# Performance work log

Hardware: AMD Instinct MI355X
Metric: run time of the kernel (lower is better)

The kernel has to match this reference:

```python
import jax, jax.numpy as jnp
import numpy as np

D = 3            # input_ch (pos dims)
L = 16           # n_levels
F = 2            # n_feats per level
LOG2 = 19
CAP = 1 << LOG2  # hashmap capacity per level
COARSEST, FINEST = 16.0, 2048.0
N = 524288
D1 = D + 1
HASH_MULT = np.int32(2531011)


def _elevate_matrix():
    # Linear map R^D -> hyperplane {sum=0} in R^{D+1} (Adams et al. permutohedral lattice)
    sf = 1.0 / np.sqrt(np.arange(1, D + 1, dtype=np.float64) * np.arange(2, D + 2, dtype=np.float64))
    E = np.zeros((D1, D), np.float32)
    E[0, :] = sf
    for i in range(1, D1):
        E[i, i - 1] = -i * sf[i - 1]
        E[i, i:] = sf[i:]
    return E


def _scales():
    g = (FINEST / COARSEST) ** (np.arange(L, dtype=np.float64) / (L - 1))
    return (COARSEST * g).astype(np.float32)


def permuto_forward(pos, params):
    E = jnp.asarray(_elevate_matrix())
    scales = jnp.asarray(_scales())
    x = pos[None] * scales[:, None, None]              # [L,N,D]
    elev = jnp.einsum('vp,lnp->lnv', E, x)             # [L,N,D1]
    # nearest lattice remainder-0 point (multiples of D1)
    rem0f = jnp.round(elev / D1) * D1
    sums = (jnp.sum(rem0f, -1) / D1).astype(jnp.int32)  # exactly integer
    di = elev - rem0f
    # rank[i] = #{j : d_j > d_i  or (d_j == d_i and j < i)}
    gt = di[..., None, :] > di[..., :, None]
    eq = di[..., None, :] == di[..., :, None]
    jlt = jnp.arange(D1)[None, :] < jnp.arange(D1)[:, None]
    rank = jnp.sum(gt | (eq & jlt), -1).astype(jnp.int32) + sums[..., None]
    rem0 = rem0f.astype(jnp.int32)
    under = (rank < 0).astype(jnp.int32)
    over = (rank > D).astype(jnp.int32)
    rank = rank + (under - over) * D1
    rem0 = rem0 + (under - over) * D1
    # barycentric weights of the D1 simplex vertices
    delta = (elev - rem0.astype(elev.dtype)) / D1      # [L,N,D1]
    dbr = jnp.take_along_axis(delta, jnp.argsort(rank, -1), -1)  # delta ordered by rank
    w0 = 1.0 + dbr[..., -1] - dbr[..., 0]
    w = jnp.concatenate([w0[..., None], -(dbr[..., 1:] - dbr[..., :-1])[..., ::-1]], -1)  # [L,N,D1]
    # integer keys of the D1 simplex vertices (first D coords; last is implicit)
    kk = jnp.arange(D1, dtype=jnp.int32)
    keys = (rem0[..., None, :D] + kk[:, None]
            - D1 * (rank[..., None, :D] > (D - kk[:, None])).astype(jnp.int32))  # [L,N,D1,D]
    # hash: k = (k + key_i) * 2531011, wrap in 32 bits, mask to capacity (pow2)
    h = jnp.zeros(keys.shape[:-1], jnp.int32)
    for i in range(D):
        h = (h + keys[..., i]) * HASH_MULT
    idx = h & (CAP - 1)                                # [L,N,D1]
    flat_idx = idx + jnp.arange(L, dtype=jnp.int32)[:, None, None] * CAP
    feats = params.reshape(L * CAP, F)[flat_idx]       # [L,N,D1,F]
    out = jnp.einsum('lnv,lnvf->lnf', w, feats)        # [L,N,F]
    return jnp.moveaxis(out, 0, 1).reshape(pos.shape[0], L * F)


def setup_inputs() -> dict:
    key = jax.random.key(0)
    k1, k2 = jax.random.split(key)
    pos = jax.random.uniform(k1, (N, D), jnp.float32)                 # coords in [0,1)
    params = jax.random.normal(k2, (L * CAP * F,), jnp.float32) * 1e-4  # param_init std
    return {"input": pos, "flattened_params": params}


def reference(input, flattened_params):
    return permuto_forward(input, flattened_params)
```

## Files before the change

kernel.cpp:

```cpp
#include <hip/hip_runtime.h>
#include <hip/hip_fp16.h>
#include <cmath>

namespace {

typedef float    vf4 __attribute__((ext_vector_type(4)));
typedef unsigned uv2 __attribute__((ext_vector_type(2)));

constexpr int kN = 524288;
constexpr int kL = 16;
constexpr int kCapLog2 = 19;
constexpr int kCap = 1 << kCapLog2;
constexpr int kCapMask = kCap - 1;
constexpr unsigned kHashMult = 2531011u;

constexpr int cD[4][3]   = {{ 8, 8, 6},{10,10, 9},{13,12,10},{17,16,14}};
constexpr int cB[4][3]   = {{-4,-16,-16},{-4,-20,-24},{-4,-24,-28},{-4,-32,-40}};
constexpr int cOff[4]    = {0, 1536, 5136, 11376};
constexpr int kLdsCnt    = 11376;
constexpr int kDenseCnt  = 26608;

constexpr int kMegaMain  = 15360;
constexpr int kBuildBlks = 104;
constexpr int kConvBaseF4 = 7 * (kCap * 2 / 4);

struct ScaleArr { float s[kL]; };

__device__ __forceinline__ void permuto_point(
    float x0, float x1, float x2, int rem0[4], int rank[4], float w[4])
{
    const float E00 = (float)( 0.70710678118654752440);
    const float E01 = (float)( 0.40824829046386301637);
    const float E02 = (float)( 0.28867513459481288225);
    const float E10 = (float)(-0.70710678118654752440);
    const float E21 = (float)(-2.0 * 0.40824829046386301637);
    const float E32 = (float)(-3.0 * 0.28867513459481288225);

    float elev[4];
    elev[0] = E00 * x0 + E01 * x1 + E02 * x2;
    elev[1] = E10 * x0 + E01 * x1 + E02 * x2;
    elev[2] =            E21 * x1 + E02 * x2;
    elev[3] =                       E32 * x2;

    float rem0f[4], di[4];
    #pragma unroll
    for (int v = 0; v < 4; ++v) {
        rem0f[v] = rintf(elev[v] * 0.25f) * 4.0f;
        di[v]    = elev[v] - rem0f[v];
    }
    const int sums = (int)((((rem0f[0] + rem0f[1]) + rem0f[2]) + rem0f[3]) * 0.25f);

    #pragma unroll
    for (int a = 0; a < 4; ++a) {
        int r = 0;
        #pragma unroll
        for (int b = 0; b < 4; ++b)
            r += (di[b] > di[a]) || (di[b] == di[a] && b < a);
        rank[a] = r + sums;
        rem0[a] = (int)rem0f[a];
    }
    #pragma unroll
    for (int v = 0; v < 4; ++v) {
        if (rank[v] < 0)      { rank[v] += 4; rem0[v] += 4; }
        else if (rank[v] > 3) { rank[v] -= 4; rem0[v] -= 4; }
    }

    float dbr[4];
    #pragma unroll
    for (int v = 0; v < 4; ++v)
        dbr[rank[v] & 3] = (elev[v] - (float)rem0[v]) * 0.25f;

    w[0] = (1.0f + dbr[3]) - dbr[0];
    w[1] = dbr[2] - dbr[3];
    w[2] = dbr[1] - dbr[2];
    w[3] = dbr[0] - dbr[1];
}

__global__ __launch_bounds__(256) void mega1(
    const float* __restrict__ pos,
    const float* __restrict__ params,
    unsigned* __restrict__ tab,
    unsigned* __restrict__ out_t16,
    unsigned* __restrict__ dense,
    ScaleArr sc)
{
    const int b = blockIdx.x;
    if (b < kMegaMain) {
        const int q = b / 5, r = b % 5;
        if (r < 2) {
            const int idx   = q * 2 + r;
            const int level = 4 + (idx >> 11);
            const int n     = ((idx & 2047) << 8) + threadIdx.x;

            const float s  = sc.s[level];
            const float x0 = __builtin_nontemporal_load(pos + 3 * n + 0) * s;
            const float x1 = __builtin_nontemporal_load(pos + 3 * n + 1) * s;
            const float x2 = __builtin_nontemporal_load(pos + 3 * n + 2) * s;

            int rem0[4], rank[4];
            float w[4];
            permuto_point(x0, x1, x2, rem0, rank, w);

            const float2* __restrict__ t2 =
                (const float2*)params + ((size_t)level << kCapLog2);
            int hidx[4];
            #pragma unroll
            for (int k = 0; k < 4; ++k) {
                int h = 0;
                #pragma unroll
                for (int i = 0; i < 3; ++i) {
                    const int key = rem0[i] + k - 4 * (rank[i] > 3 - k);
                    h = (int)((unsigned)(h + key) * kHashMult);
                }
                hidx[k] = h & kCapMask;
            }
            float2 f[4];
            #pragma unroll
            for (int k = 0; k < 4; ++k) f[k] = t2[hidx[k]];

            float o0 = 0.0f, o1 = 0.0f;
            #pragma unroll
            for (int k = 0; k < 4; ++k) { o0 += w[k] * f[k].x; o1 += w[k] * f[k].y; }

            const __half2 po = __floats2half2_rn(o0, o1);
            __builtin_nontemporal_store(*reinterpret_cast<const unsigned*>(&po),
                                        out_t16 + ((size_t)level << kCapLog2) + n);
        } else {
            const int i  = q * 3 + (r - 2);
            const int jj = kConvBaseF4 + i * 256 + threadIdx.x;
            vf4 v = __builtin_nontemporal_load((const vf4*)params + jj);
            __half2 a = __floats2half2_rn(v.x, v.y);
            __half2 c = __floats2half2_rn(v.z, v.w);
            uv2 o;
            o.x = *reinterpret_cast<unsigned*>(&a);
            o.y = *reinterpret_cast<unsigned*>(&c);
            __builtin_nontemporal_store(o, (uv2*)tab + jj);
        }
    } else {
        const int e = (b - kMegaMain) * 256 + threadIdx.x;
        if (e >= kDenseCnt) return;
        int l, r;
        if      (e < cOff[1]) { l = 0; r = e; }
        else if (e < cOff[2]) { l = 1; r = e - cOff[1]; }
        else if (e < cOff[3]) { l = 2; r = e - cOff[2]; }
        else                  { l = 3; r = e - cOff[3]; }
        const int d0 = cD[l][0], d1 = cD[l][1], d2 = cD[l][2];
        const int per = d0 * d1 * d2;
        int rr = r;
        const int k  = rr / per;  rr -= k * per;
        const int i0 = rr / (d1 * d2); rr -= i0 * (d1 * d2);
        const int i1 = rr / d2;
        const int i2 = rr - i1 * d2;

        const int key0 = cB[l][0] + 4 * i0 + k;
        const int key1 = cB[l][1] + 4 * i1 + k;
        const int key2 = cB[l][2] + 4 * i2 + k;
        int h = 0;
        h = (int)((unsigned)(h + key0) * kHashMult);
        h = (int)((unsigned)(h + key1) * kHashMult);
        h = (int)((unsigned)(h + key2) * kHashMult);
        const size_t entry = ((size_t)l << kCapLog2) + (h & kCapMask);
        const __half2 hv = __floats2half2_rn(params[entry * 2], params[entry * 2 + 1]);
        dense[e] = *reinterpret_cast<const unsigned*>(&hv);
    }
}

__global__ __launch_bounds__(256) void fine715(
    const float* __restrict__ pos,
    const unsigned* __restrict__ tab,
    unsigned* __restrict__ out_t16,
    ScaleArr sc)
{
    const int b   = blockIdx.x;
    const int xcd = b & 7;
    const int j   = b >> 3;
    int level, n;
    if (j < 2048) {
        level = 7 + xcd;
        n = (j << 8) + threadIdx.x;
    } else {
        level = 15;
        const int c = (j - 2048) + (xcd << 8);
        n = (c << 8) + threadIdx.x;
    }

    const float s  = sc.s[level];
    const float x0 = __builtin_nontemporal_load(pos + 3 * n + 0) * s;
    const float x1 = __builtin_nontemporal_load(pos + 3 * n + 1) * s;
    const float x2 = __builtin_nontemporal_load(pos + 3 * n + 2) * s;

    int rem0[4], rank[4];
    float w[4];
    permuto_point(x0, x1, x2, rem0, rank, w);

    const unsigned* __restrict__ t = tab + ((size_t)level << kCapLog2);
    int hidx[4];
    #pragma unroll
    for (int k = 0; k < 4; ++k) {
        int h = 0;
        #pragma unroll
        for (int i = 0; i < 3; ++i) {
            const int key = rem0[i] + k - 4 * (rank[i] > 3 - k);
            h = (int)((unsigned)(h + key) * kHashMult);
        }
        hidx[k] = h & kCapMask;
    }
    unsigned e[4];
    #pragma unroll
    for (int k = 0; k < 4; ++k) e[k] = t[hidx[k]];

    float o0 = 0.0f, o1 = 0.0f;
    #pragma unroll
    for (int k = 0; k < 4; ++k) {
        const __half2 hv = *reinterpret_cast<const __half2*>(&e[k]);
        o0 += w[k] * __low2float(hv);
        o1 += w[k] * __high2float(hv);
    }
    const __half2 po = __floats2half2_rn(o0, o1);
    __builtin_nontemporal_store(*reinterpret_cast<const unsigned*>(&po),
                                out_t16 + ((size_t)level << kCapLog2) + n);
}

__global__ __launch_bounds__(256) void permuto_coarse(
    const float* __restrict__ pos,
    const unsigned* __restrict__ dense,
    unsigned* __restrict__ out_t16,
    ScaleArr sc)
{
    __shared__ unsigned sd[kLdsCnt];
    for (int i = threadIdx.x; i < kLdsCnt; i += 256)
        sd[i] = dense[i];
    __syncthreads();

    const int n = blockIdx.x * 256 + threadIdx.x;
    const float p0 = __builtin_nontemporal_load(pos + 3 * n + 0);
    const float p1 = __builtin_nontemporal_load(pos + 3 * n + 1);
    const float p2 = __builtin_nontemporal_load(pos + 3 * n + 2);
    const unsigned* __restrict__ denseL3 = dense + cOff[3];

    #pragma unroll
    for (int l = 0; l < 4; ++l) {
        const float s = sc.s[l];
        int rem0[4], rank[4];
        float w[4];
        permuto_point(p0 * s, p1 * s, p2 * s, rem0, rank, w);

        unsigned ev[4];
        #pragma unroll
        for (int k = 0; k < 4; ++k) {
            const int i0 = (rem0[0] - 4 * (rank[0] > 3 - k) - cB[l][0]) >> 2;
            const int i1 = (rem0[1] - 4 * (rank[1] > 3 - k) - cB[l][1]) >> 2;
            const int i2 = (rem0[2] - 4 * (rank[2] > 3 - k) - cB[l][2]) >> 2;
            const int idx = ((k * cD[l][0] + i0) * cD[l][1] + i1) * cD[l][2] + i2;
            ev[k] = (l < 3) ? sd[cOff[l] + idx] : denseL3[idx];
        }
        float o0 = 0.0f, o1 = 0.0f;
        #pragma unroll
        for (int k = 0; k < 4; ++k) {
            const __half2 hv = *reinterpret_cast<const __half2*>(&ev[k]);
            o0 += w[k] * __low2float(hv);
            o1 += w[k] * __high2float(hv);
        }
        const __half2 po = __floats2half2_rn(o0, o1);
        __builtin_nontemporal_store(*reinterpret_cast<const unsigned*>(&po),
                                    out_t16 + ((size_t)l << kCapLog2) + n);
    }
}

__global__ __launch_bounds__(256) void transpose_out16(
    const unsigned* __restrict__ out_t16, vf4* __restrict__ out4)
{
    __shared__ float tile[256][36];
    const int t  = threadIdx.x;
    const int p0 = blockIdx.x * 256;

    #pragma unroll
    for (int l = 0; l < kL; ++l) {
        const unsigned u = __builtin_nontemporal_load(out_t16 + ((size_t)l << kCapLog2) + p0 + t);
        const __half2 hv = *reinterpret_cast<const __half2*>(&u);
        tile[t][2 * l + 0] = __low2float(hv);
        tile[t][2 * l + 1] = __high2float(hv);
    }
    __syncthreads();

    const size_t base = (size_t)p0 * 8;
    #pragma unroll
    for (int i = 0; i < 8; ++i) {
        const int idx = i * 256 + t;
        const int p = idx >> 3, q = idx & 7;
        vf4 v = *reinterpret_cast<const vf4*>(&tile[p][4 * q]);
        out4[base + idx] = v;
    }
}

__global__ __launch_bounds__(256) void permuto_fwd(
    const float* __restrict__ pos,
    const float* __restrict__ params,
    float* __restrict__ out,
    ScaleArr sc)
{
    const int gid = blockIdx.x * 256 + threadIdx.x;
    const int l = gid & (kL - 1);
    const int n = gid >> 4;

    const float s  = sc.s[l];
    const float x0 = pos[3 * n + 0] * s;
    const float x1 = pos[3 * n + 1] * s;
    const float x2 = pos[3 * n + 2] * s;

    int rem0[4], rank[4];
    float w[4];
    permuto_point(x0, x1, x2, rem0, rank, w);

    const float2* __restrict__ tab = (const float2*)params + ((size_t)l << kCapLog2);
    float o0 = 0.0f, o1 = 0.0f;
    #pragma unroll
    for (int k = 0; k < 4; ++k) {
        int h = 0;
        #pragma unroll
        for (int i = 0; i < 3; ++i) {
            const int key = rem0[i] + k - 4 * (rank[i] > 3 - k);
            h = (int)((unsigned)(h + key) * kHashMult);
        }
        const float2 f = tab[h & kCapMask];
        o0 += w[k] * f.x;
        o1 += w[k] * f.y;
    }
    ((float2*)out)[(n << 4) + l] = make_float2(o0, o1);
}

}

extern "C" void kernel_launch(void* const* d_in, const int* in_sizes, int n_in,
                              void* d_out, int out_size, void* d_ws, size_t ws_size,
                              hipStream_t stream) {
    const float* pos    = (const float*)d_in[0];
    const float* params = (const float*)d_in[1];
    float* out          = (float*)d_out;

    ScaleArr sc;
    for (int l = 0; l < kL; ++l)
        sc.s[l] = (float)(16.0 * pow(128.0, (double)l / 15.0));

    const size_t tab_bytes   = (size_t)kL * kCap * 4;
    const size_t outt_bytes  = (size_t)kL * kN * 4;
    const size_t dense_bytes = (size_t)kDenseCnt * 4;

    if (ws_size >= tab_bytes + outt_bytes + dense_bytes) {
        unsigned* tab     = (unsigned*)d_ws;
        unsigned* out_t16 = (unsigned*)((char*)d_ws + tab_bytes);
        unsigned* dense   = (unsigned*)((char*)d_ws + tab_bytes + outt_bytes);

        mega1<<<kMegaMain + kBuildBlks, 256, 0, stream>>>(pos, params, tab, out_t16, dense, sc);
        fine715<<<8 * 2304, 256, 0, stream>>>(pos, tab, out_t16, sc);
        permuto_coarse<<<kN / 256, 256, 0, stream>>>(pos, dense, out_t16, sc);
        transpose_out16<<<kN / 256, 256, 0, stream>>>(out_t16, (vf4*)out);
    } else {
        permuto_fwd<<<(kN * kL) / 256, 256, 0, stream>>>(pos, params, out, sc);
    }
}
```

Measured before the change: 175.1 us.

## Split fine gathers into halves and overlap transpose with second-half gathers

The three launches for fine gathers, coarse gathers and transpose become a split by point halves. The first kernel runs the fine levels and coarse levels for the first half plus level 15 for that half. The second kernel runs the fine gathers for the second half alongside the transpose of the first half. A final small kernel transposes the second half. The aim is to overlap the bandwidth-bound transpose with the latency-bound random gathers and to cut tail effects between launches, at the cost of a larger LDS footprint per block in the combined kernels, which could lower occupancy.

New measurement: 177.2 us. Within noise of the previous version (+1.2%).

```diff
diff --git a/kernel.cpp b/kernel.cpp
--- a/kernel.cpp
+++ b/kernel.cpp
@@ -13,6 +13,9 @@
 constexpr int kCap = 1 << kCapLog2;
 constexpr int kCapMask = kCap - 1;
 constexpr unsigned kHashMult = 2531011u;
+
+constexpr int kHalf = kN / 2;
+constexpr int kHB   = kHalf / 256;
 
 constexpr int cD[4][3]   = {{ 8, 8, 6},{10,10, 9},{13,12,10},{17,16,14}};
 constexpr int cB[4][3]   = {{-4,-16,-16},{-4,-20,-24},{-4,-24,-28},{-4,-32,-40}};
@@ -74,6 +77,47 @@
     w[1] = dbr[2] - dbr[3];
     w[2] = dbr[1] - dbr[2];
     w[3] = dbr[0] - dbr[1];
+}
+
+__device__ __forceinline__ void fine_job(
+    const float* __restrict__ pos, const unsigned* __restrict__ tab,
+    unsigned* __restrict__ out_t16, const ScaleArr& sc, int level, int n)
+{
+    const float s  = sc.s[level];
+    const float x0 = __builtin_nontemporal_load(pos + 3 * n + 0) * s;
+    const float x1 = __builtin_nontemporal_load(pos + 3 * n + 1) * s;
+    const float x2 = __builtin_nontemporal_load(pos + 3 * n + 2) * s;
+
+    int rem0[4], rank[4];
+    float w[4];
+    permuto_point(x0, x1, x2, rem0, rank, w);
+
+    const unsigned* __restrict__ t = tab + ((size_t)level << kCapLog2);
+    int hidx[4];
+    #pragma unroll
+    for (int k = 0; k < 4; ++k) {
+        int h = 0;
+        #pragma unroll
+        for (int i = 0; i < 3; ++i) {
+            const int key = rem0[i] + k - 4 * (rank[i] > 3 - k);
+            h = (int)((unsigned)(h + key) * kHashMult);
+        }
+        hidx[k] = h & kCapMask;
+    }
+    unsigned e[4];
+    #pragma unroll
+    for (int k = 0; k < 4; ++k) e[k] = t[hidx[k]];
+
+    float o0 = 0.0f, o1 = 0.0f;
+    #pragma unroll
+    for (int k = 0; k < 4; ++k) {
+        const __half2 hv = *reinterpret_cast<const __half2*>(&e[k]);
+        o0 += w[k] * __low2float(hv);
+        o1 += w[k] * __high2float(hv);
+    }
+    const __half2 po = __floats2half2_rn(o0, o1);
+    __builtin_nontemporal_store(*reinterpret_cast<const unsigned*>(&po),
+                                out_t16 + ((size_t)level << kCapLog2) + n);
 }
 
 __global__ __launch_bounds__(256) void mega1(
@@ -165,114 +209,72 @@
     }
 }
 
-__global__ __launch_bounds__(256) void fine715(
+__global__ __launch_bounds__(256) void gather_a(
     const float* __restrict__ pos,
     const unsigned* __restrict__ tab,
-    unsigned* __restrict__ out_t16,
-    ScaleArr sc)
-{
-    const int b   = blockIdx.x;
-    const int xcd = b & 7;
-    const int j   = b >> 3;
-    int level, n;
-    if (j < 2048) {
-        level = 7 + xcd;
-        n = (j << 8) + threadIdx.x;
-    } else {
-        level = 15;
-        const int c = (j - 2048) + (xcd << 8);
-        n = (c << 8) + threadIdx.x;
-    }
-
-    const float s  = sc.s[level];
-    const float x0 = __builtin_nontemporal_load(pos + 3 * n + 0) * s;
-    const float x1 = __builtin_nontemporal_load(pos + 3 * n + 1) * s;
-    const float x2 = __builtin_nontemporal_load(pos + 3 * n + 2) * s;
-
-    int rem0[4], rank[4];
-    float w[4];
-    permuto_point(x0, x1, x2, rem0, rank, w);
-
-    const unsigned* __restrict__ t = tab + ((size_t)level << kCapLog2);
-    int hidx[4];
-    #pragma unroll
-    for (int k = 0; k < 4; ++k) {
-        int h = 0;
-        #pragma unroll
-        for (int i = 0; i < 3; ++i) {
-            const int key = rem0[i] + k - 4 * (rank[i] > 3 - k);
-            h = (int)((unsigned)(h + key) * kHashMult);
-        }
-        hidx[k] = h & kCapMask;
-    }
-    unsigned e[4];
-    #pragma unroll
-    for (int k = 0; k < 4; ++k) e[k] = t[hidx[k]];
-
-    float o0 = 0.0f, o1 = 0.0f;
-    #pragma unroll
-    for (int k = 0; k < 4; ++k) {
-        const __half2 hv = *reinterpret_cast<const __half2*>(&e[k]);
-        o0 += w[k] * __low2float(hv);
-        o1 += w[k] * __high2float(hv);
-    }
-    const __half2 po = __floats2half2_rn(o0, o1);
-    __builtin_nontemporal_store(*reinterpret_cast<const unsigned*>(&po),
-                                out_t16 + ((size_t)level << kCapLog2) + n);
-}
-
-__global__ __launch_bounds__(256) void permuto_coarse(
-    const float* __restrict__ pos,
     const unsigned* __restrict__ dense,
     unsigned* __restrict__ out_t16,
     ScaleArr sc)
 {
-    __shared__ unsigned sd[kLdsCnt];
-    for (int i = threadIdx.x; i < kLdsCnt; i += 256)
-        sd[i] = dense[i];
-    __syncthreads();
-
-    const int n = blockIdx.x * 256 + threadIdx.x;
-    const float p0 = __builtin_nontemporal_load(pos + 3 * n + 0);
-    const float p1 = __builtin_nontemporal_load(pos + 3 * n + 1);
-    const float p2 = __builtin_nontemporal_load(pos + 3 * n + 2);
-    const unsigned* __restrict__ denseL3 = dense + cOff[3];
-
-    #pragma unroll
-    for (int l = 0; l < 4; ++l) {
-        const float s = sc.s[l];
-        int rem0[4], rank[4];
-        float w[4];
-        permuto_point(p0 * s, p1 * s, p2 * s, rem0, rank, w);
-
-        unsigned ev[4];
+    __shared__ unsigned shbuf[kLdsCnt];
+    const int b = blockIdx.x;
+
+    if (b < 8 * kHB) {
+        const int level = 7 + (b & 7);
+        const int n = ((b >> 3) << 8) + threadIdx.x;
+        fine_job(pos, tab, out_t16, sc, level, n);
+    } else if (b < 8 * kHB + 2048) {
+        for (int i = threadIdx.x; i < kLdsCnt; i += 256)
+            shbuf[i] = dense[i];
+        __syncthreads();
+
+        const int n = (b - 8 * kHB) * 256 + threadIdx.x;
+        const float p0 = __builtin_nontemporal_load(pos + 3 * n + 0);
+        const float p1 = __builtin_nontemporal_load(pos + 3 * n + 1);
+        const float p2 = __builtin_nontemporal_load(pos + 3 * n + 2);
+        const unsigned* __restrict__ denseL3 = dense + cOff[3];
+
         #pragma unroll
-        for (int k = 0; k < 4; ++k) {
-            const int i0 = (rem0[0] - 4 * (rank[0] > 3 - k) - cB[l][0]) >> 2;
-            const int i1 = (rem0[1] - 4 * (rank[1] > 3 - k) - cB[l][1]) >> 2;
-            const int i2 = (rem0[2] - 4 * (rank[2] > 3 - k) - cB[l][2]) >> 2;
-            const int idx = ((k * cD[l][0] + i0) * cD[l][1] + i1) * cD[l][2] + i2;
-            ev[k] = (l < 3) ? sd[cOff[l] + idx] : denseL3[idx];
+        for (int l = 0; l < 4; ++l) {
+            const float s = sc.s[l];
+            int rem0[4], rank[4];
+            float w[4];
+            permuto_point(p0 * s, p1 * s, p2 * s, rem0, rank, w);
+
+            unsigned ev[4];
+            #pragma unroll
+            for (int k = 0; k < 4; ++k) {
+                const int i0 = (rem0[0] - 4 * (rank[0] > 3 - k) - cB[l][0]) >> 2;
+                const int i1 = (rem0[1] - 4 * (rank[1] > 3 - k) - cB[l][1]) >> 2;
+                const int i2 = (rem0[2] - 4 * (rank[2] > 3 - k) - cB[l][2]) >> 2;
+                const int idx = ((k * cD[l][0] + i0) * cD[l][1] + i1) * cD[l][2] + i2;
+                ev[k] = (l < 3) ? shbuf[cOff[l] + idx] : denseL3[idx];
+            }
+            float o0 = 0.0f, o1 = 0.0f;
+            #pragma unroll
+            for (int k = 0; k < 4; ++k) {
+                const __half2 hv = *reinterpret_cast<const __half2*>(&ev[k]);
+                o0 += w[k] * __low2float(hv);
+                o1 += w[k] * __high2float(hv);
+            }
+            const __half2 po = __floats2half2_rn(o0, o1);
+            __builtin_nontemporal_store(*reinterpret_cast<const unsigned*>(&po),
+                                        out_t16 + ((size_t)l << kCapLog2) + n);
         }
-        float o0 = 0.0f, o1 = 0.0f;
-        #pragma unroll
-        for (int k = 0; k < 4; ++k) {
-            const __half2 hv = *reinterpret_cast<const __half2*>(&ev[k]);
-            o0 += w[k] * __low2float(hv);
-            o1 += w[k] * __high2float(hv);
-        }
-        const __half2 po = __floats2half2_rn(o0, o1);
-        __builtin_nontemporal_store(*reinterpret_cast<const unsigned*>(&po),
-                                    out_t16 + ((size_t)l << kCapLog2) + n);
-    }
-}
-
-__global__ __launch_bounds__(256) void transpose_out16(
-    const unsigned* __restrict__ out_t16, vf4* __restrict__ out4)
-{
-    __shared__ float tile[256][36];
+    } else {
+        const int q = b - (8 * kHB + 2048);
+        const int c = (q >> 3) + ((q & 7) << 7);
+        const int n = (c << 8) + threadIdx.x;
+        fine_job(pos, tab, out_t16, sc, 15, n);
+    }
+}
+
+__device__ __forceinline__ void transpose_job(
+    const unsigned* __restrict__ out_t16, vf4* __restrict__ out4,
+    int pb, float (*tile)[36])
+{
     const int t  = threadIdx.x;
-    const int p0 = blockIdx.x * 256;
+    const int p0 = pb * 256;
 
     #pragma unroll
     for (int l = 0; l < kL; ++l) {
@@ -291,6 +293,38 @@
         vf4 v = *reinterpret_cast<const vf4*>(&tile[p][4 * q]);
         out4[base + idx] = v;
     }
+}
+
+__global__ __launch_bounds__(256) void gather_b(
+    const float* __restrict__ pos,
+    const unsigned* __restrict__ tab,
+    const unsigned* __restrict__ out_t16c,
+    unsigned* __restrict__ out_t16,
+    vf4* __restrict__ out4,
+    ScaleArr sc)
+{
+    __shared__ float tile[256][36];
+    const int b = blockIdx.x;
+
+    if (b < 8 * kHB) {
+        const int level = 7 + (b & 7);
+        const int n = ((b >> 3) << 8) + threadIdx.x + kHalf;
+        fine_job(pos, tab, out_t16, sc, level, n);
+    } else if (b < 9 * kHB) {
+        const int q = b - 8 * kHB;
+        const int c = (q >> 3) + ((q & 7) << 7);
+        const int n = (c << 8) + threadIdx.x + kHalf;
+        fine_job(pos, tab, out_t16, sc, 15, n);
+    } else {
+        transpose_job(out_t16c, out4, b - 9 * kHB, tile);
+    }
+}
+
+__global__ __launch_bounds__(256) void transpose_b(
+    const unsigned* __restrict__ out_t16, vf4* __restrict__ out4)
+{
+    __shared__ float tile[256][36];
+    transpose_job(out_t16, out4, blockIdx.x + kHB, tile);
 }
 
 __global__ __launch_bounds__(256) void permuto_fwd(
@@ -352,9 +386,9 @@
         unsigned* dense   = (unsigned*)((char*)d_ws + tab_bytes + outt_bytes);
 
         mega1<<<kMegaMain + kBuildBlks, 256, 0, stream>>>(pos, params, tab, out_t16, dense, sc);
-        fine715<<<8 * 2304, 256, 0, stream>>>(pos, tab, out_t16, sc);
-        permuto_coarse<<<kN / 256, 256, 0, stream>>>(pos, dense, out_t16, sc);
-        transpose_out16<<<kN / 256, 256, 0, stream>>>(out_t16, (vf4*)out);
+        gather_a<<<8 * kHB + 2048 + kHB, 256, 0, stream>>>(pos, tab, dense, out_t16, sc);
+        gather_b<<<9 * kHB + kHB, 256, 0, stream>>>(pos, tab, out_t16, out_t16, (vf4*)out, sc);
+        transpose_b<<<kHB, 256, 0, stream>>>(out_t16, (vf4*)out);
     } else {
         permuto_fwd<<<(kN * kL) / 256, 256, 0, stream>>>(pos, params, out, sc);
     }
```

## Merge coarse-level pass into fine-level kernel and shrink transpose LDS tile

Applied to the files above, without the earlier changes.

Folds the coarse levels 0-3 work into the fine-level kernel as extra blocks, so one launch covers both. The coarse path now reads the dense table straight from global/L2 instead of staging it in LDS. This drops a kernel launch and the per-block LDS fill, and the merged kernel gets an occupancy hint. The transpose now stores packed half2 values in a smaller LDS tile and converts to float when writing out, which cuts LDS footprint and traffic but makes the output writes less contiguous.

New measurement: 168.5 us. 3.7% less time.

```diff
diff --git a/kernel.cpp b/kernel.cpp
--- a/kernel.cpp
+++ b/kernel.cpp
@@ -17,12 +17,16 @@
 constexpr int cD[4][3]   = {{ 8, 8, 6},{10,10, 9},{13,12,10},{17,16,14}};
 constexpr int cB[4][3]   = {{-4,-16,-16},{-4,-20,-24},{-4,-24,-28},{-4,-32,-40}};
 constexpr int cOff[4]    = {0, 1536, 5136, 11376};
-constexpr int kLdsCnt    = 11376;
 constexpr int kDenseCnt  = 26608;
 
 constexpr int kMegaMain  = 15360;
 constexpr int kBuildBlks = 104;
 constexpr int kConvBaseF4 = 7 * (kCap * 2 / 4);
+
+constexpr int kPB        = kN / 256;
+constexpr int kFinePrim  = 8 * kPB;
+constexpr int kFineTail  = kPB;
+constexpr int kCoarseBlk = kPB;
 
 struct ScaleArr { float s[kL]; };
 
@@ -74,6 +78,47 @@
     w[1] = dbr[2] - dbr[3];
     w[2] = dbr[1] - dbr[2];
     w[3] = dbr[0] - dbr[1];
+}
+
+__device__ __forceinline__ void fine_job(
+    const float* __restrict__ pos, const unsigned* __restrict__ tab,
+    unsigned* __restrict__ out_t16, const ScaleArr& sc, int level, int n)
+{
+    const float s  = sc.s[level];
+    const float x0 = __builtin_nontemporal_load(pos + 3 * n + 0) * s;
+    const float x1 = __builtin_nontemporal_load(pos + 3 * n + 1) * s;
+    const float x2 = __builtin_nontemporal_load(pos + 3 * n + 2) * s;
+
+    int rem0[4], rank[4];
+    float w[4];
+    permuto_point(x0, x1, x2, rem0, rank, w);
+
+    const unsigned* __restrict__ t = tab + ((size_t)level << kCapLog2);
+    int hidx[4];
+    #pragma unroll
+    for (int k = 0; k < 4; ++k) {
+        int h = 0;
+        #pragma unroll
+        for (int i = 0; i < 3; ++i) {
+            const int key = rem0[i] + k - 4 * (rank[i] > 3 - k);
+            h = (int)((unsigned)(h + key) * kHashMult);
+        }
+        hidx[k] = h & kCapMask;
+    }
+    unsigned e[4];
+    #pragma unroll
+    for (int k = 0; k < 4; ++k) e[k] = t[hidx[k]];
+
+    float o0 = 0.0f, o1 = 0.0f;
+    #pragma unroll
+    for (int k = 0; k < 4; ++k) {
+        const __half2 hv = *reinterpret_cast<const __half2*>(&e[k]);
+        o0 += w[k] * __low2float(hv);
+        o1 += w[k] * __high2float(hv);
+    }
+    const __half2 po = __floats2half2_rn(o0, o1);
+    __builtin_nontemporal_store(*reinterpret_cast<const unsigned*>(&po),
+                                out_t16 + ((size_t)level << kCapLog2) + n);
 }
 
 __global__ __launch_bounds__(256) void mega1(
@@ -165,36 +210,114 @@
     }
 }
 
-__global__ __launch_bounds__(256) void fine715(
+__global__ __launch_bounds__(256, 8) void fine715c(
     const float* __restrict__ pos,
     const unsigned* __restrict__ tab,
+    const unsigned* __restrict__ dense,
     unsigned* __restrict__ out_t16,
     ScaleArr sc)
 {
-    const int b   = blockIdx.x;
-    const int xcd = b & 7;
-    const int j   = b >> 3;
-    int level, n;
-    if (j < 2048) {
-        level = 7 + xcd;
-        n = (j << 8) + threadIdx.x;
+    const int b = blockIdx.x;
+
+    if (b < kFinePrim) {
+        const int level = 7 + (b & 7);
+        const int n = ((b >> 3) << 8) + threadIdx.x;
+        fine_job(pos, tab, out_t16, sc, level, n);
+    } else if (b < kFinePrim + kFineTail) {
+        const int q = b - kFinePrim;
+        const int c = (q >> 3) + ((q & 7) << 8);
+        const int n = (c << 8) + threadIdx.x;
+        fine_job(pos, tab, out_t16, sc, 15, n);
     } else {
-        level = 15;
-        const int c = (j - 2048) + (xcd << 8);
-        n = (c << 8) + threadIdx.x;
-    }
-
-    const float s  = sc.s[level];
-    const float x0 = __builtin_nontemporal_load(pos + 3 * n + 0) * s;
-    const float x1 = __builtin_nontemporal_load(pos + 3 * n + 1) * s;
-    const float x2 = __builtin_nontemporal_load(pos + 3 * n + 2) * s;
+        const int n = (b - kFinePrim - kFineTail) * 256 + threadIdx.x;
+        const float p0 = __builtin_nontemporal_load(pos + 3 * n + 0);
+        const float p1 = __builtin_nontemporal_load(pos + 3 * n + 1);
+        const float p2 = __builtin_nontemporal_load(pos + 3 * n + 2);
+
+        #pragma unroll 1
+        for (int l = 0; l < 4; ++l) {
+            const float s = sc.s[l];
+            int rem0[4], rank[4];
+            float w[4];
+            permuto_point(p0 * s, p1 * s, p2 * s, rem0, rank, w);
+
+            const unsigned* __restrict__ dl = dense + cOff[l];
+            unsigned ev[4];
+            #pragma unroll
+            for (int k = 0; k < 4; ++k) {
+                const int i0 = (rem0[0] - 4 * (rank[0] > 3 - k) - cB[l][0]) >> 2;
+                const int i1 = (rem0[1] - 4 * (rank[1] > 3 - k) - cB[l][1]) >> 2;
+                const int i2 = (rem0[2] - 4 * (rank[2] > 3 - k) - cB[l][2]) >> 2;
+                ev[k] = dl[((k * cD[l][0] + i0) * cD[l][1] + i1) * cD[l][2] + i2];
+            }
+            float o0 = 0.0f, o1 = 0.0f;
+            #pragma unroll
+            for (int k = 0; k < 4; ++k) {
+                const __half2 hv = *reinterpret_cast<const __half2*>(&ev[k]);
+                o0 += w[k] * __low2float(hv);
+                o1 += w[k] * __high2float(hv);
+            }
+            const __half2 po = __floats2half2_rn(o0, o1);
+            __builtin_nontemporal_store(*reinterpret_cast<const unsigned*>(&po),
+                                        out_t16 + ((size_t)l << kCapLog2) + n);
+        }
+    }
+}
+
+__global__ __launch_bounds__(256) void transpose16(
+    const unsigned* __restrict__ out_t16, vf4* __restrict__ out4)
+{
+    __shared__ unsigned tile[256][17];
+    const int t  = threadIdx.x;
+    const int p0 = blockIdx.x * 256;
+
+    #pragma unroll
+    for (int l = 0; l < kL; ++l)
+        tile[t][l] = __builtin_nontemporal_load(out_t16 + ((size_t)l << kCapLog2) + p0 + t);
+    __syncthreads();
+
+    const size_t base = (size_t)p0 * 8;
+    #pragma unroll
+    for (int j = 0; j < 4; ++j) {
+        const int idx = j * 256 + t;
+        const int p = idx >> 2, q = idx & 3;
+        float f[8];
+        #pragma unroll
+        for (int i = 0; i < 4; ++i) {
+            const unsigned u = tile[p][4 * q + i];
+            const __half2 hv = *reinterpret_cast<const __half2*>(&u);
+            f[2 * i + 0] = __low2float(hv);
+            f[2 * i + 1] = __high2float(hv);
+        }
+        vf4 a, c;
+        a.x = f[0]; a.y = f[1]; a.z = f[2]; a.w = f[3];
+        c.x = f[4]; c.y = f[5]; c.z = f[6]; c.w = f[7];
+        out4[base + (size_t)p * 8 + 2 * q + 0] = a;
+        out4[base + (size_t)p * 8 + 2 * q + 1] = c;
+    }
+}
+
+__global__ __launch_bounds__(256) void permuto_fwd(
+    const float* __restrict__ pos,
+    const float* __restrict__ params,
+    float* __restrict__ out,
+    ScaleArr sc)
+{
+    const int gid = blockIdx.x * 256 + threadIdx.x;
+    const int l = gid & (kL - 1);
+    const int n = gid >> 4;
+
+    const float s  = sc.s[l];
+    const float x0 = pos[3 * n + 0] * s;
+    const float x1 = pos[3 * n + 1] * s;
+    const float x2 = pos[3 * n + 2] * s;
 
     int rem0[4], rank[4];
     float w[4];
     permuto_point(x0, x1, x2, rem0, rank, w);
 
-    const unsigned* __restrict__ t = tab + ((size_t)level << kCapLog2);
-    int hidx[4];
+    const float2* __restrict__ tab = (const float2*)params + ((size_t)l << kCapLog2);
+    float o0 = 0.0f, o1 = 0.0f;
     #pragma unroll
     for (int k = 0; k < 4; ++k) {
         int h = 0;
@@ -203,125 +326,6 @@
             const int key = rem0[i] + k - 4 * (rank[i] > 3 - k);
             h = (int)((unsigned)(h + key) * kHashMult);
         }
-        hidx[k] = h & kCapMask;
-    }
-    unsigned e[4];
-    #pragma unroll
-    for (int k = 0; k < 4; ++k) e[k] = t[hidx[k]];
-
-    float o0 = 0.0f, o1 = 0.0f;
-    #pragma unroll
-    for (int k = 0; k < 4; ++k) {
-        const __half2 hv = *reinterpret_cast<const __half2*>(&e[k]);
-        o0 += w[k] * __low2float(hv);
-        o1 += w[k] * __high2float(hv);
-    }
-    const __half2 po = __floats2half2_rn(o0, o1);
-    __builtin_nontemporal_store(*reinterpret_cast<const unsigned*>(&po),
-                                out_t16 + ((size_t)level << kCapLog2) + n);
-}
-
-__global__ __launch_bounds__(256) void permuto_coarse(
-    const float* __restrict__ pos,
-    const unsigned* __restrict__ dense,
-    unsigned* __restrict__ out_t16,
-    ScaleArr sc)
-{
-    __shared__ unsigned sd[kLdsCnt];
-    for (int i = threadIdx.x; i < kLdsCnt; i += 256)
-        sd[i] = dense[i];
-    __syncthreads();
-
-    const int n = blockIdx.x * 256 + threadIdx.x;
-    const float p0 = __builtin_nontemporal_load(pos + 3 * n + 0);
-    const float p1 = __builtin_nontemporal_load(pos + 3 * n + 1);
-    const float p2 = __builtin_nontemporal_load(pos + 3 * n + 2);
-    const unsigned* __restrict__ denseL3 = dense + cOff[3];
-
-    #pragma unroll
-    for (int l = 0; l < 4; ++l) {
-        const float s = sc.s[l];
-        int rem0[4], rank[4];
-        float w[4];
-        permuto_point(p0 * s, p1 * s, p2 * s, rem0, rank, w);
-
-        unsigned ev[4];
-        #pragma unroll
-        for (int k = 0; k < 4; ++k) {
-            const int i0 = (rem0[0] - 4 * (rank[0] > 3 - k) - cB[l][0]) >> 2;
-            const int i1 = (rem0[1] - 4 * (rank[1] > 3 - k) - cB[l][1]) >> 2;
-            const int i2 = (rem0[2] - 4 * (rank[2] > 3 - k) - cB[l][2]) >> 2;
-            const int idx = ((k * cD[l][0] + i0) * cD[l][1] + i1) * cD[l][2] + i2;
-            ev[k] = (l < 3) ? sd[cOff[l] + idx] : denseL3[idx];
-        }
-        float o0 = 0.0f, o1 = 0.0f;
-        #pragma unroll
-        for (int k = 0; k < 4; ++k) {
-            const __half2 hv = *reinterpret_cast<const __half2*>(&ev[k]);
-            o0 += w[k] * __low2float(hv);
-            o1 += w[k] * __high2float(hv);
-        }
-        const __half2 po = __floats2half2_rn(o0, o1);
-        __builtin_nontemporal_store(*reinterpret_cast<const unsigned*>(&po),
-                                    out_t16 + ((size_t)l << kCapLog2) + n);
-    }
-}
-
-__global__ __launch_bounds__(256) void transpose_out16(
-    const unsigned* __restrict__ out_t16, vf4* __restrict__ out4)
-{
-    __shared__ float tile[256][36];
-    const int t  = threadIdx.x;
-    const int p0 = blockIdx.x * 256;
-
-    #pragma unroll
-    for (int l = 0; l < kL; ++l) {
-        const unsigned u = __builtin_nontemporal_load(out_t16 + ((size_t)l << kCapLog2) + p0 + t);
-        const __half2 hv = *reinterpret_cast<const __half2*>(&u);
-        tile[t][2 * l + 0] = __low2float(hv);
-        tile[t][2 * l + 1] = __high2float(hv);
-    }
-    __syncthreads();
-
-    const size_t base = (size_t)p0 * 8;
-    #pragma unroll
-    for (int i = 0; i < 8; ++i) {
-        const int idx = i * 256 + t;
-        const int p = idx >> 3, q = idx & 7;
-        vf4 v = *reinterpret_cast<const vf4*>(&tile[p][4 * q]);
-        out4[base + idx] = v;
-    }
-}
-
-__global__ __launch_bounds__(256) void permuto_fwd(
-    const float* __restrict__ pos,
-    const float* __restrict__ params,
-    float* __restrict__ out,
-    ScaleArr sc)
-{
-    const int gid = blockIdx.x * 256 + threadIdx.x;
-    const int l = gid & (kL - 1);
-    const int n = gid >> 4;
-
-    const float s  = sc.s[l];
-    const float x0 = pos[3 * n + 0] * s;
-    const float x1 = pos[3 * n + 1] * s;
-    const float x2 = pos[3 * n + 2] * s;
-
-    int rem0[4], rank[4];
-    float w[4];
-    permuto_point(x0, x1, x2, rem0, rank, w);
-
-    const float2* __restrict__ tab = (const float2*)params + ((size_t)l << kCapLog2);
-    float o0 = 0.0f, o1 = 0.0f;
-    #pragma unroll
-    for (int k = 0; k < 4; ++k) {
-        int h = 0;
-        #pragma unroll
-        for (int i = 0; i < 3; ++i) {
-            const int key = rem0[i] + k - 4 * (rank[i] > 3 - k);
-            h = (int)((unsigned)(h + key) * kHashMult);
-        }
         const float2 f = tab[h & kCapMask];
         o0 += w[k] * f.x;
         o1 += w[k] * f.y;
@@ -352,9 +356,8 @@
         unsigned* dense   = (unsigned*)((char*)d_ws + tab_bytes + outt_bytes);
 
         mega1<<<kMegaMain + kBuildBlks, 256, 0, stream>>>(pos, params, tab, out_t16, dense, sc);
-        fine715<<<8 * 2304, 256, 0, stream>>>(pos, tab, out_t16, sc);
-        permuto_coarse<<<kN / 256, 256, 0, stream>>>(pos, dense, out_t16, sc);
-        transpose_out16<<<kN / 256, 256, 0, stream>>>(out_t16, (vf4*)out);
+        fine715c<<<kFinePrim + kFineTail + kCoarseBlk, 256, 0, stream>>>(pos, tab, dense, out_t16, sc);
+        transpose16<<<kN / 256, 256, 0, stream>>>(out_t16, (vf4*)out);
     } else {
         permuto_fwd<<<(kN * kL) / 256, 256, 0, stream>>>(pos, params, out, sc);
     }
```
